# Kernel tuning notes

Hardware: AMD Instinct MI355X
Metric: run time of the kernel (lower is better)

The kernel has to match this reference:

```python
import jax, jax.numpy as jnp
import numpy as np

N_NODES = 1_000_000
N_EDGES = 16_000_000
ALPHA = 0.85
MAX_ITER = 100
TOL = 1e-6


def setup_inputs() -> dict:
    key = jax.random.key(0)
    k1, k2 = jax.random.split(key)
    x = jax.random.normal(k1, (N_NODES,), dtype=jnp.float32)
    edge_index = jax.random.randint(k2, (2, N_EDGES), 0, N_NODES, dtype=jnp.int64)
    return {"x": x, "edge_index": edge_index}


def reference(x, edge_index):
    N = x.shape[0]
    rows = edge_index[0]  # destination (row index of sparse M)
    cols = edge_index[1]  # source (column index; out-degree normalization)

    # values of M*alpha: alpha / out_degree(col), gathered per edge
    deg = jax.ops.segment_sum(jnp.ones_like(cols, dtype=jnp.float32), cols,
                              num_segments=N)  # torch.bincount(columns)
    vals = ALPHA / deg[cols]  # [E]; div-by-zero -> inf, matching torch

    inv_n = jnp.float32(1.0) / N
    teleport = (1.0 - ALPHA) * inv_n
    v0 = jnp.full((N,), inv_n, dtype=jnp.float32)
    thresh = jnp.float32(N) * TOL

    def step(carry, _):
        v, done = carry
        # SpMV: out[row] += vals * v[col]
        new_v = jax.ops.segment_sum(vals * v[cols], rows, num_segments=N) + teleport
        err = jnp.abs(new_v - v).sum()
        v_next = jnp.where(done, v, new_v)
        done_next = done | (err < thresh)
        return (v_next, done_next), None

    (v, _), _ = jax.lax.scan(step, (v0, jnp.array(False)), None, length=MAX_ITER)
    return v
```

## Files before the change

kernel.cpp:

```cpp
#include <hip/hip_runtime.h>
#include <hip/hip_cooperative_groups.h>

namespace cg = cooperative_groups;


static constexpr int   NN       = 1000000;
static constexpr int   NE       = 16000000;
static constexpr float ALPHA    = 0.85f;
static constexpr int   MAX_ITER = 100;
static constexpr float THRESH   = 1.0f;
static constexpr float INV_N    = 1.0f / 1000000.0f;
static constexpr float TELEPORT = 0.15f * (1.0f / 1000000.0f);
static constexpr float SCALE    = 8796093022208.0f;
static constexpr float INVSCALE = 1.0f / 8796093022208.0f;

static constexpr int T     = 256;
static constexpr int NCH   = 2048;
static constexpr int BSH   = 14;
static constexpr int BKN   = 16384;
static constexpr int NBK   = 64;
static constexpr int NSUBB = 496;
static constexpr int NSLC  = 489;

static constexpr size_t OFF_WCG  = 0;
static constexpr size_t OFF_COLP = 0;
static constexpr size_t OFF_HP   = 32001024;
static constexpr size_t OFF_WRG  = 64002048;
static constexpr size_t OFF_PACC = 96003072;
static constexpr size_t OFF_CNTR = 128508928;
static constexpr size_t OFF_CNTC = 129033216;
static constexpr size_t OFF_CTRL = 129557504;
static constexpr size_t OFF_RDEG = 129561600;
static constexpr size_t OFF_W    = 133561600;
static constexpr size_t NEED     = 137561632;

typedef int      vi4 __attribute__((ext_vector_type(4)));
typedef unsigned vu4 __attribute__((ext_vector_type(4)));

template<typename TT>
__device__ __forceinline__ TT ntload(const TT* p) { return __builtin_nontemporal_load(p); }

struct P {
    unsigned* wcg; unsigned short* colp; unsigned short* hpart; unsigned short* wrg;
    int* pacc; unsigned* cntR; unsigned* cntC;
    float* rdeg; float* w;
    unsigned* totR; unsigned* totC; unsigned* baseR; unsigned* baseC;
    unsigned* flags; int* ovf; float* errF;
};
__device__ __forceinline__ P mk(char* ws) {
    P p;
    p.wcg  = (unsigned*)(ws + OFF_WCG);
    p.colp = (unsigned short*)(ws + OFF_COLP);
    p.hpart= (unsigned short*)(ws + OFF_HP);
    p.wrg  = (unsigned short*)(ws + OFF_WRG);
    p.pacc = (int*)(ws + OFF_PACC);
    p.cntR = (unsigned*)(ws + OFF_CNTR);
    p.cntC = (unsigned*)(ws + OFF_CNTC);
    unsigned* ctrl = (unsigned*)(ws + OFF_CTRL);
    p.rdeg = (float*)(ws + OFF_RDEG);
    p.w    = (float*)(ws + OFF_W);
    p.totR = ctrl; p.totC = ctrl + 64; p.baseR = ctrl + 128; p.baseC = ctrl + 200;
    p.flags = ctrl + 280; p.ovf = (int*)(ctrl + 281); p.errF = (float*)(ctrl + 288);
    return p;
}

__device__ void atomic_fallback(cg::grid_group& grid, int is64,
                                const int* e32, const long long* e64,
                                int* ai, int* deg, float* rdeg,
                                float* vA, float* vB, float* w,
                                float* err, float* out,
                                int tid, int stride, int th)
{
    for (int i = tid; i < NN; i += stride) { ai[i] = 0; deg[i] = 0; vA[i] = INV_N; }
    grid.sync();
    if (is64) { const long long* cols = e64 + NE;
        for (int e = tid; e < NE; e += stride) atomicAdd(&deg[(int)cols[e]], 1); }
    else      { const int* cols = e32 + NE;
        for (int e = tid; e < NE; e += stride) atomicAdd(&deg[cols[e]], 1); }
    grid.sync();
    for (int i = tid; i < NN; i += stride) rdeg[i] = ALPHA / (float)deg[i];
    grid.sync();
    float* v = vA; float* nv = vB;
    for (int iter = 0; iter < MAX_ITER; ++iter) {
        for (int i = tid; i < NN; i += stride) { w[i] = v[i] * rdeg[i]; ai[i] = 0; }
        grid.sync();
        if (is64) { const long long* rows = e64; const long long* cols = e64 + NE;
            for (int e = tid; e < NE; e += stride)
                atomicAdd(&ai[(int)rows[e]], __float2int_rn(w[(int)cols[e]] * SCALE)); }
        else { const int* rows = e32; const int* cols = e32 + NE;
            for (int e = tid; e < NE; e += stride)
                atomicAdd(&ai[rows[e]], __float2int_rn(w[cols[e]] * SCALE)); }
        grid.sync();
        float pe = 0.0f;
        for (int i = tid; i < NN; i += stride) {
            float x = TELEPORT + (float)ai[i] * INVSCALE;
            pe += fabsf(x - v[i]); nv[i] = x;
        }
        #pragma unroll
        for (int off = 32; off > 0; off >>= 1) pe += __shfl_down(pe, off, 64);
        if ((th & 63) == 0) unsafeAtomicAdd(&err[iter], pe);
        grid.sync();
        float e = ((volatile float*)err)[iter];
        float* t = v; v = nv; nv = t;
        if (e < THRESH) break;
    }
    for (int i = tid; i < NN; i += stride) out[i] = v[i];
}

__global__ __launch_bounds__(256) void k0_init(const int* __restrict__ e32, char* ws)
{
    P p = mk(ws);
    __shared__ int snz;
    const int th = threadIdx.x;
    if (th == 0) snz = 0;
    __syncthreads();
    if (e32[2 * th + 1] != 0) atomicOr(&snz, 1);
    __syncthreads();
    if (th == 0) { p.flags[0] = (snz == 0) ? 1u : 0u; *p.ovf = 0; p.w[NN] = 0.0f; }
    if (th < MAX_ITER) p.errF[th] = 0.0f;
}

__global__ __launch_bounds__(256, 8) void k1_hist(const int* __restrict__ e32, char* ws)
{
    P p = mk(ws);
    if (p.flags[0]) return;
    __shared__ int h[128];
    const int th = threadIdx.x, blk = blockIdx.x;
    const int e0 = (int)(((long long)NE * blk) >> 11);
    const int e1 = (int)(((long long)NE * (blk + 1)) >> 11);
    if (th < 128) h[th] = 0;
    __syncthreads();
    const vi4* R4 = (const vi4*)e32;
    const vi4* C4 = (const vi4*)(e32 + NE);
    const int qe = (e1 + 3) >> 2;
    for (int q = (e0 >> 2) + th; q < qe; q += T) {
        vi4 R = R4[q], C = C4[q];
        int rr[4] = {R.x, R.y, R.z, R.w}, cc[4] = {C.x, C.y, C.z, C.w};
        #pragma unroll
        for (int j = 0; j < 4; ++j) {
            int e = 4 * q + j;
            if (e >= e0 && e < e1) {
                atomicAdd(&h[rr[j] >> BSH], 1);
                atomicAdd(&h[64 + (cc[j] >> BSH)], 1);
            }
        }
    }
    __syncthreads();
    if (th < 64) {
        p.cntR[(size_t)th * NCH + blk] = (unsigned)h[th];
        p.cntC[(size_t)th * NCH + blk] = (unsigned)h[64 + th];
    }
}

__global__ __launch_bounds__(256, 4) void k2_scan(char* ws)
{
    P p = mk(ws);
    if (p.flags[0]) return;
    __shared__ int S[256];
    const int th = threadIdx.x, blk = blockIdx.x;
    const int side = blk >> 6, b = blk & 63;
    unsigned* cnt = (side ? p.cntC : p.cntR) + (size_t)b * NCH;
    unsigned v[8]; unsigned s = 0;
    #pragma unroll
    for (int i = 0; i < 8; ++i) { v[i] = cnt[8 * th + i]; s += v[i]; }
    S[th] = (int)s; __syncthreads();
    for (int off = 1; off < 256; off <<= 1) {
        int x = (th >= off) ? S[th - off] : 0;
        __syncthreads(); S[th] += x; __syncthreads();
    }
    unsigned run = (unsigned)S[th] - s;
    #pragma unroll
    for (int i = 0; i < 8; ++i) { unsigned t = v[i]; cnt[8 * th + i] = run; run += t; }
    if (th == 255) (side ? p.totC : p.totR)[b] = run;
}

__global__ __launch_bounds__(256) void k2b_bases(char* ws)
{
    P p = mk(ws);
    if (p.flags[0]) return;
    __shared__ int S[128];
    const int th = threadIdx.x;
    unsigned pt = 0;
    if (th < 128) {
        unsigned t = (th < 64) ? p.totR[th] : p.totC[th - 64];
        pt = (t + 7u) & ~7u;
        S[th] = (int)pt;
    }
    __syncthreads();
    for (int off = 1; off < 64; off <<= 1) {
        int x = (th < 128 && (th & 63) >= off) ? S[th - off] : 0;
        __syncthreads(); if (th < 128) S[th] += x; __syncthreads();
    }
    if (th < 64) {
        p.baseR[th] = (unsigned)S[th] - pt;
        if (th == 63) p.baseR[64] = (unsigned)S[63];
    } else if (th < 128) {
        p.baseC[th - 64] = (unsigned)S[th] - pt;
        if (th == 127) p.baseC[64] = (unsigned)S[127];
    }
    __syncthreads();
    if (th < 64) {
        unsigned tot = p.totC[th], bs = p.baseC[th], pp = (tot + 7u) & ~7u;
        for (unsigned i = tot; i < pp; ++i) p.colp[bs + i] = 0;
    }
}

__global__ __launch_bounds__(256, 6) void k3a_col(const int* __restrict__ e32, char* ws)
{
    P p = mk(ws);
    if (p.flags[0]) return;
    __shared__ int SH3[4288];
    unsigned short* pcL = (unsigned short*)SH3;
    int* fills = SH3 + 4096; int* flsh = SH3 + 4160; int* wpos = SH3 + 4224;
    const int th = threadIdx.x, blk = blockIdx.x;
    if (th < 64) { fills[th] = 0; flsh[th] = 0;
                   wpos[th] = (int)(p.baseC[th] + p.cntC[(size_t)th * NCH + blk]); }
    __syncthreads();
    const int e0 = (int)(((long long)NE * blk) >> 11);
    const int e1 = (int)(((long long)NE * (blk + 1)) >> 11);
    const vi4* C4 = (const vi4*)(e32 + NE);
    const int qs = e0 >> 2, qe = (e1 + 3) >> 2;
    vi4 Ccur = {0, 0, 0, 0}; if (qs + th < qe) Ccur = C4[qs + th];
    for (int qb = qs; qb < qe; qb += T) {
        vi4 Cnext = {0, 0, 0, 0};
        { int qn = qb + T + th; if (qn < qe) Cnext = C4[qn]; }
        const int q = qb + th;
        if (q < qe) {
            int cc[4] = {Ccur.x, Ccur.y, Ccur.z, Ccur.w};
            #pragma unroll
            for (int j = 0; j < 4; ++j) {
                int e = 4 * q + j;
                if (e >= e0 && e < e1) {
                    int bb = cc[j] >> BSH;
                    int idx = atomicAdd(&fills[bb], 1);
                    pcL[bb * 128 + (idx & 127)] = (unsigned short)(cc[j] & (BKN - 1));
                }
            }
        }
        __syncthreads();
        const int wv = th >> 6, lane = th & 63;
        for (int k = 0; k < 16; ++k) {
            const int b = wv * 16 + k;
            int ff = fills[b], fl = flsh[b], wp = wpos[b];
            if (ff - fl > 128) *p.ovf = 1;
            while (ff - fl >= 64) {
                p.colp[wp + lane] = pcL[b * 128 + ((fl + lane) & 127)];
                fl += 64; wp += 64;
            }
            if (lane == 0) { flsh[b] = fl; wpos[b] = wp; }
        }
        __syncthreads();
        Ccur = Cnext;
    }
    {
        const int wv = th >> 6, lane = th & 63;
        for (int k = 0; k < 16; ++k) {
            const int b = wv * 16 + k;
            int ff = fills[b], fl = flsh[b], wp = wpos[b];
            while (ff > fl) {
                int n = min(64, ff - fl);
                if (lane < n) p.colp[wp + lane] = pcL[b * 128 + ((fl + lane) & 127)];
                fl += n; wp += n;
            }
        }
    }
}

__global__ __launch_bounds__(256, 2) void k4a_deg(char* ws)
{
    P p = mk(ws);
    if (p.flags[0] || *p.ovf) return;
    __shared__ int SH[16384];
    const int th = threadIdx.x, blk = blockIdx.x;
    const int b = blk >> 3, sub = blk & 7;
    for (int j = th; j < 16384; j += T) SH[j] = 0;
    __syncthreads();
    const unsigned bs = p.baseC[b], tot = p.totC[b], pt = (tot + 7u) & ~7u;
    const unsigned nq = pt >> 3;
    const unsigned qlo = (nq * (unsigned)sub) >> 3;
    const unsigned qhi = (nq * (unsigned)(sub + 1)) >> 3;
    const vu4* p8 = (const vu4*)p.colp + (bs >> 3);
    for (unsigned q = qlo + th; q < qhi; q += T) {
        vu4 x = ntload(p8 + q);
        atomicAdd(&SH[x.x & 0xFFFFu], 1); atomicAdd(&SH[x.x >> 16], 1);
        atomicAdd(&SH[x.y & 0xFFFFu], 1); atomicAdd(&SH[x.y >> 16], 1);
        atomicAdd(&SH[x.z & 0xFFFFu], 1); atomicAdd(&SH[x.z >> 16], 1);
        atomicAdd(&SH[x.w & 0xFFFFu], 1); atomicAdd(&SH[x.w >> 16], 1);
    }
    __syncthreads();
    unsigned* hp = (unsigned*)(p.hpart + (size_t)blk * 16384);
    for (int j = th; j < 8192; j += T)
        __builtin_nontemporal_store(
            (unsigned)((SH[2*j] & 0xFFFF) | (SH[2*j+1] << 16)), hp + j);
}

__global__ __launch_bounds__(256, 8) void k4b_merge(char* ws)
{
    P p = mk(ws);
    if (p.flags[0] || *p.ovf) return;
    const int th = threadIdx.x, blk = blockIdx.x;
    const int b = blk >> 3, off = (blk & 7) * 2048;
    const unsigned padC = ((p.totC[b] + 7u) & ~7u) - p.totC[b];
    for (int j = th; j < 1024; j += T) {
        unsigned lo = 0, hi = 0;
        #pragma unroll
        for (int q = 0; q < 8; ++q) {
            const unsigned* hp = (const unsigned*)(p.hpart + (size_t)(b*8+q)*16384 + off);
            unsigned x = ntload(hp + j);
            lo += x & 0xFFFFu; hi += x >> 16;
        }
        if (off == 0 && j == 0) lo -= padC;
        int node = b * BKN + off + 2 * j;
        if (node < NN) {
            float r0 = ALPHA / (float)(int)lo;
            float r1 = ALPHA / (float)(int)hi;
            float2 rr = {r0, r1};
            *(float2*)&p.rdeg[node] = rr;
            float2 ww = {INV_N * r0, INV_N * r1};
            *(float2*)&p.w[node] = ww;
        }
    }
}

__global__ __launch_bounds__(256, 3) void k3b_row(const int* __restrict__ e32, char* ws)
{
    P p = mk(ws);
    if (p.flags[0] || *p.ovf) return;
    __shared__ int SH3[12480];
    int*            wcL = SH3;
    unsigned short* wrL = (unsigned short*)(SH3 + 8192);
    int* fills = SH3 + 12288; int* flsh = SH3 + 12352; int* wpos = SH3 + 12416;
    const int th = threadIdx.x, blk = blockIdx.x;
    if (blk < 64 && th == 0) {
        unsigned tot = p.totR[blk], bs = p.baseR[blk], pt = (tot + 7u) & ~7u;
        for (unsigned i = tot; i < pt; ++i) { p.wcg[bs + i] = (unsigned)NN; p.wrg[bs + i] = 0; }
    }
    if (th < 64) { fills[th] = 0; flsh[th] = 0;
                   wpos[th] = (int)(p.baseR[th] + p.cntR[(size_t)th * NCH + blk]); }
    __syncthreads();
    const int e0 = (int)(((long long)NE * blk) >> 11);
    const int e1 = (int)(((long long)NE * (blk + 1)) >> 11);
    const vi4* R4 = (const vi4*)e32;
    const vi4* C4 = (const vi4*)(e32 + NE);
    const int qs = e0 >> 2, qe = (e1 + 3) >> 2;
    vi4 Rcur = {0,0,0,0}, Ccur = {0,0,0,0};
    if (qs + th < qe) { Rcur = R4[qs + th]; Ccur = C4[qs + th]; }
    for (int qb = qs; qb < qe; qb += T) {
        vi4 Rnext = {0,0,0,0}, Cnext = {0,0,0,0};
        { int qn = qb + T + th; if (qn < qe) { Rnext = R4[qn]; Cnext = C4[qn]; } }
        const int q = qb + th;
        if (q < qe) {
            int rr[4] = {Rcur.x, Rcur.y, Rcur.z, Rcur.w};
            int cc[4] = {Ccur.x, Ccur.y, Ccur.z, Ccur.w};
            #pragma unroll
            for (int j = 0; j < 4; ++j) {
                int e = 4 * q + j;
                if (e >= e0 && e < e1) {
                    int bb = rr[j] >> BSH;
                    int idx = atomicAdd(&fills[bb], 1);
                    int sl = idx & 127;
                    wcL[bb * 128 + sl] = cc[j];
                    wrL[bb * 128 + sl] = (unsigned short)(rr[j] & (BKN - 1));
                }
            }
        }
        __syncthreads();
        const int wv = th >> 6, lane = th & 63;
        for (int k = 0; k < 16; ++k) {
            const int b = wv * 16 + k;
            int ff = fills[b], fl = flsh[b], wp = wpos[b];
            if (ff - fl > 128) *p.ovf = 1;
            while (ff - fl >= 64) {
                p.wcg[wp + lane] = (unsigned)wcL[b * 128 + ((fl + lane) & 127)];
                p.wrg[wp + lane] = wrL[b * 128 + ((fl + lane) & 127)];
                fl += 64; wp += 64;
            }
            if (lane == 0) { flsh[b] = fl; wpos[b] = wp; }
        }
        __syncthreads();
        Rcur = Rnext; Ccur = Cnext;
    }
    {
        const int wv = th >> 6, lane = th & 63;
        for (int k = 0; k < 16; ++k) {
            const int b = wv * 16 + k;
            int ff = fills[b], fl = flsh[b], wp = wpos[b];
            while (ff > fl) {
                int n = min(64, ff - fl);
                if (lane < n) {
                    p.wcg[wp + lane] = (unsigned)wcL[b * 128 + ((fl + lane) & 127)];
                    p.wrg[wp + lane] = wrL[b * 128 + ((fl + lane) & 127)];
                }
                fl += n; wp += n;
            }
        }
    }
}

__global__ __launch_bounds__(256, 2)
void k5_iter(const int* __restrict__ e32, const long long* __restrict__ e64,
             char* __restrict__ ws, float* __restrict__ out)
{
    cg::grid_group grid = cg::this_grid();
    P p = mk(ws);
    const int th = threadIdx.x, blk = blockIdx.x;
    const int tid = blk * T + th;
    const int stride = gridDim.x * T;
    __shared__ int SH[16384];
    __shared__ float sred[4];

    if (p.flags[0] || *p.ovf) {
        atomic_fallback(grid, (int)p.flags[0], e32, e64,
                        (int*)ws, (int*)(ws + (size_t)4*1024*1024), p.rdeg,
                        (float*)(ws + (size_t)8*1024*1024),
                        (float*)(ws + (size_t)12*1024*1024),
                        (float*)(ws + (size_t)16*1024*1024),
                        p.errF, out, tid, stride, th);
        return;
    }

    for (int iter = 0; iter < MAX_ITER; ++iter) {
        if (blk < NSUBB) {
            const int b = blk >> 3, sub = blk & 7;
            for (int j = th; j < 16384; j += T) SH[j] = 0;
            __syncthreads();
            const unsigned bs = p.baseR[b], tot = p.totR[b], pt = (tot + 7u) & ~7u;
            const unsigned nq = pt >> 3;
            const unsigned qlo = (nq * (unsigned)sub) >> 3;
            const unsigned qhi = (nq * (unsigned)(sub + 1)) >> 3;
            const vu4* r8 = (const vu4*)p.wrg + (bs >> 3);
            const vi4* c8 = (const vi4*)p.wcg + (bs >> 2);
            for (unsigned q = qlo + th; q < qhi; q += T) {
                vu4 rl = ntload(r8 + q);
                vi4 ca = ntload(c8 + 2*q), cb = ntload(c8 + 2*q + 1);
                atomicAdd(&SH[rl.x & 0xFFFFu], __float2int_rn(p.w[(unsigned)ca.x] * SCALE));
                atomicAdd(&SH[rl.x >> 16],     __float2int_rn(p.w[(unsigned)ca.y] * SCALE));
                atomicAdd(&SH[rl.y & 0xFFFFu], __float2int_rn(p.w[(unsigned)ca.z] * SCALE));
                atomicAdd(&SH[rl.y >> 16],     __float2int_rn(p.w[(unsigned)ca.w] * SCALE));
                atomicAdd(&SH[rl.z & 0xFFFFu], __float2int_rn(p.w[(unsigned)cb.x] * SCALE));
                atomicAdd(&SH[rl.z >> 16],     __float2int_rn(p.w[(unsigned)cb.y] * SCALE));
                atomicAdd(&SH[rl.w & 0xFFFFu], __float2int_rn(p.w[(unsigned)cb.z] * SCALE));
                atomicAdd(&SH[rl.w >> 16],     __float2int_rn(p.w[(unsigned)cb.w] * SCALE));
            }
            __syncthreads();
            vi4* pa = (vi4*)(p.pacc + (size_t)blk * 16384);
            const vi4* s4 = (const vi4*)SH;
            for (int j = th; j < 4096; j += T)
                __builtin_nontemporal_store(s4[j], pa + j);
        }
        grid.sync();

        float pe = 0.0f;
        if (blk < NSLC) {
            const int b = blk >> 3, off = (blk & 7) * 2048;
            for (int g = th; g < 512; g += T) {
                int node = b * BKN + off + 4 * g;
                if (node < NN) {
                    vi4 acc = {0, 0, 0, 0};
                    #pragma unroll
                    for (int q = 0; q < 8; ++q) {
                        const vi4* pp = (const vi4*)(p.pacc + (size_t)(b*8+q)*16384 + off);
                        vi4 x = ntload(pp + g);
                        acc.x += x.x; acc.y += x.y; acc.z += x.z; acc.w += x.w;
                    }
                    float x0 = TELEPORT + (float)acc.x * INVSCALE;
                    float x1 = TELEPORT + (float)acc.y * INVSCALE;
                    float x2 = TELEPORT + (float)acc.z * INVSCALE;
                    float x3 = TELEPORT + (float)acc.w * INVSCALE;
                    float4 prev;
                    if (iter == 0) prev = make_float4(INV_N, INV_N, INV_N, INV_N);
                    else           prev = *(const float4*)&out[node];
                    pe += fabsf(x0 - prev.x) + fabsf(x1 - prev.y)
                        + fabsf(x2 - prev.z) + fabsf(x3 - prev.w);
                    float4 nv = {x0, x1, x2, x3};
                    *(float4*)&out[node] = nv;
                    float4 rd = *(const float4*)&p.rdeg[node];
                    float4 nw = {x0*rd.x, x1*rd.y, x2*rd.z, x3*rd.w};
                    *(float4*)&p.w[node] = nw;
                }
            }
            #pragma unroll
            for (int o2 = 32; o2 > 0; o2 >>= 1) pe += __shfl_down(pe, o2, 64);
            if ((th & 63) == 0) sred[th >> 6] = pe;
            __syncthreads();
            if (th == 0)
                unsafeAtomicAdd(&p.errF[iter], sred[0] + sred[1] + sred[2] + sred[3]);
        }
        grid.sync();
        const float e = ((volatile float*)p.errF)[iter];
        if (e < THRESH) break;
    }
}

__global__ __launch_bounds__(256, 4)
void pagerank_atomic(const int* __restrict__ e32, const long long* __restrict__ e64,
                     int* __restrict__ ai, int* __restrict__ deg,
                     float* __restrict__ rdeg, float* __restrict__ vA,
                     float* __restrict__ vB, float* __restrict__ w,
                     float* __restrict__ err, int* __restrict__ flags,
                     float* __restrict__ out)
{
    cg::grid_group grid = cg::this_grid();
    const int tid = blockIdx.x * blockDim.x + threadIdx.x;
    const int stride = gridDim.x * blockDim.x;
    if (tid < MAX_ITER) err[tid] = 0.0f;
    if (tid == 0) {
        int nz = 0;
        for (int k = 1; k < 512; k += 2) nz |= e32[k];
        flags[0] = (nz == 0) ? 1 : 0;
    }
    grid.sync();
    atomic_fallback(grid, flags[0], e32, e64, ai, deg, rdeg, vA, vB, w, err, out,
                    tid, stride, threadIdx.x);
}

extern "C" void kernel_launch(void* const* d_in, const int* in_sizes, int n_in,
                              void* d_out, int out_size, void* d_ws, size_t ws_size,
                              hipStream_t stream)
{
    (void)n_in; (void)out_size; (void)in_sizes;
    const int*       e32 = (const int*)d_in[1];
    const long long* e64 = (const long long*)d_in[1];
    float* out = (float*)d_out;
    char*  ws  = (char*)d_ws;

    int occ = 0;
    hipOccupancyMaxActiveBlocksPerMultiprocessor(&occ, (const void*)k5_iter, T, 0);

    if (ws_size >= NEED && occ >= 2) {
        k0_init<<<1,    T, 0, stream>>>(e32, ws);
        k1_hist<<<NCH,  T, 0, stream>>>(e32, ws);
        k2_scan<<<128,  T, 0, stream>>>(ws);
        k2b_bases<<<1,  T, 0, stream>>>(ws);
        k3a_col<<<NCH,  T, 0, stream>>>(e32, ws);
        k4a_deg<<<NSUBB,T, 0, stream>>>(ws);
        k4b_merge<<<NSLC,T,0, stream>>>(ws);
        k3b_row<<<NCH,  T, 0, stream>>>(e32, ws);
        void* args[] = { (void*)&e32, (void*)&e64, (void*)&ws, (void*)&out };
        hipLaunchCooperativeKernel((const void*)k5_iter,
                                   dim3(512), dim3(T), args, 0, stream);
        return;
    }

    const size_t MB = 1024 * 1024;
    int*   ai    = (int*)(ws);
    int*   deg   = (int*)(ws + 4 * MB);
    float* rdeg  = (float*)(ws + 8 * MB);
    float* vA    = (float*)(ws + 12 * MB);
    float* vB    = (float*)(ws + 16 * MB);
    float* w     = (float*)(ws + 20 * MB);
    float* err   = (float*)(ws + 24 * MB);
    int*   flg   = (int*)(ws + 24 * MB + 4096);
    int occ2 = 0;
    hipOccupancyMaxActiveBlocksPerMultiprocessor(&occ2, (const void*)pagerank_atomic, 256, 0);
    if (occ2 < 1) occ2 = 1;
    int grid = occ2 * 256; if (grid > 2048) grid = 2048;
    void* args[] = { (void*)&e32, (void*)&e64, (void*)&ai, (void*)&deg, (void*)&rdeg,
                     (void*)&vA, (void*)&vB, (void*)&w, (void*)&err, (void*)&flg,
                     (void*)&out };
    hipLaunchCooperativeKernel((const void*)pagerank_atomic,
                               dim3(grid), dim3(256), args, 0, stream);
}
```

Baseline: 618.3 us.

## Compute out-degrees with global atomics and software-pipeline the SpMV gather loop

Replaces the multi-kernel column bucketing pipeline (column partitioning, per-bucket shared histograms and a merge) with direct global atomicAdd on a per-node degree array during the histogram pass, followed by a small kernel that turns the counts into reciprocal degrees and the initial weights. It also software-pipelines the SpMV inner loop in the iteration kernel, double-buffering the index loads and the w gathers so the gathers of the next chunk overlap the shared-memory atomics of the current one. Global atomics on 16M random addresses may contend or generate heavy memory traffic, and the pipelining raises register pressure in a kernel launched with occupancy bound 2.

```diff
diff --git a/kernel.cpp b/kernel.cpp
--- a/kernel.cpp
+++ b/kernel.cpp
@@ -21,10 +21,10 @@
 static constexpr int NBK   = 64;
 static constexpr int NSUBB = 496;
 static constexpr int NSLC  = 489;
+static constexpr int NDEG4 = 250000;
+static constexpr int GDEG  = 977;
 
 static constexpr size_t OFF_WCG  = 0;
-static constexpr size_t OFF_COLP = 0;
-static constexpr size_t OFF_HP   = 32001024;
 static constexpr size_t OFF_WRG  = 64002048;
 static constexpr size_t OFF_PACC = 96003072;
 static constexpr size_t OFF_CNTR = 128508928;
@@ -41,7 +41,7 @@
 __device__ __forceinline__ TT ntload(const TT* p) { return __builtin_nontemporal_load(p); }
 
 struct P {
-    unsigned* wcg; unsigned short* colp; unsigned short* hpart; unsigned short* wrg;
+    unsigned* wcg; unsigned short* wrg;
     int* pacc; unsigned* cntR; unsigned* cntC;
     float* rdeg; float* w;
     unsigned* totR; unsigned* totC; unsigned* baseR; unsigned* baseC;
@@ -50,8 +50,6 @@
 __device__ __forceinline__ P mk(char* ws) {
     P p;
     p.wcg  = (unsigned*)(ws + OFF_WCG);
-    p.colp = (unsigned short*)(ws + OFF_COLP);
-    p.hpart= (unsigned short*)(ws + OFF_HP);
     p.wrg  = (unsigned short*)(ws + OFF_WRG);
     p.pacc = (int*)(ws + OFF_PACC);
     p.cntR = (unsigned*)(ws + OFF_CNTR);
@@ -112,23 +110,31 @@
     P p = mk(ws);
     __shared__ int snz;
     const int th = threadIdx.x;
-    if (th == 0) snz = 0;
-    __syncthreads();
-    if (e32[2 * th + 1] != 0) atomicOr(&snz, 1);
-    __syncthreads();
-    if (th == 0) { p.flags[0] = (snz == 0) ? 1u : 0u; *p.ovf = 0; p.w[NN] = 0.0f; }
-    if (th < MAX_ITER) p.errF[th] = 0.0f;
+    const int idx = blockIdx.x * T + th;
+    if (idx < NDEG4) {
+        vi4 z = {0, 0, 0, 0};
+        *((vi4*)(ws + OFF_RDEG) + idx) = z;
+    }
+    if (blockIdx.x == 0) {
+        if (th == 0) snz = 0;
+        __syncthreads();
+        if (e32[2 * th + 1] != 0) atomicOr(&snz, 1);
+        __syncthreads();
+        if (th == 0) { p.flags[0] = (snz == 0) ? 1u : 0u; *p.ovf = 0; p.w[NN] = 0.0f; }
+        if (th < MAX_ITER) p.errF[th] = 0.0f;
+    }
 }
 
 __global__ __launch_bounds__(256, 8) void k1_hist(const int* __restrict__ e32, char* ws)
 {
     P p = mk(ws);
     if (p.flags[0]) return;
-    __shared__ int h[128];
+    __shared__ int h[64];
+    int* __restrict__ deg = (int*)(ws + OFF_RDEG);
     const int th = threadIdx.x, blk = blockIdx.x;
     const int e0 = (int)(((long long)NE * blk) >> 11);
     const int e1 = (int)(((long long)NE * (blk + 1)) >> 11);
-    if (th < 128) h[th] = 0;
+    if (th < 64) h[th] = 0;
     __syncthreads();
     const vi4* R4 = (const vi4*)e32;
     const vi4* C4 = (const vi4*)(e32 + NE);
@@ -141,15 +147,12 @@
             int e = 4 * q + j;
             if (e >= e0 && e < e1) {
                 atomicAdd(&h[rr[j] >> BSH], 1);
-                atomicAdd(&h[64 + (cc[j] >> BSH)], 1);
+                atomicAdd(&deg[cc[j]], 1);
             }
         }
     }
     __syncthreads();
-    if (th < 64) {
-        p.cntR[(size_t)th * NCH + blk] = (unsigned)h[th];
-        p.cntC[(size_t)th * NCH + blk] = (unsigned)h[64 + th];
-    }
+    if (th < 64) p.cntR[(size_t)th * NCH + blk] = (unsigned)h[th];
 }
 
 __global__ __launch_bounds__(256, 4) void k2_scan(char* ws)
@@ -157,9 +160,8 @@
     P p = mk(ws);
     if (p.flags[0]) return;
     __shared__ int S[256];
-    const int th = threadIdx.x, blk = blockIdx.x;
-    const int side = blk >> 6, b = blk & 63;
-    unsigned* cnt = (side ? p.cntC : p.cntR) + (size_t)b * NCH;
+    const int th = threadIdx.x, b = blockIdx.x;
+    unsigned* cnt = p.cntR + (size_t)b * NCH;
     unsigned v[8]; unsigned s = 0;
     #pragma unroll
     for (int i = 0; i < 8; ++i) { v[i] = cnt[8 * th + i]; s += v[i]; }
@@ -171,155 +173,47 @@
     unsigned run = (unsigned)S[th] - s;
     #pragma unroll
     for (int i = 0; i < 8; ++i) { unsigned t = v[i]; cnt[8 * th + i] = run; run += t; }
-    if (th == 255) (side ? p.totC : p.totR)[b] = run;
+    if (th == 255) p.totR[b] = run;
 }
 
 __global__ __launch_bounds__(256) void k2b_bases(char* ws)
 {
     P p = mk(ws);
     if (p.flags[0]) return;
-    __shared__ int S[128];
+    __shared__ int S[64];
     const int th = threadIdx.x;
     unsigned pt = 0;
-    if (th < 128) {
-        unsigned t = (th < 64) ? p.totR[th] : p.totC[th - 64];
+    if (th < 64) {
+        unsigned t = p.totR[th];
         pt = (t + 7u) & ~7u;
         S[th] = (int)pt;
     }
     __syncthreads();
     for (int off = 1; off < 64; off <<= 1) {
-        int x = (th < 128 && (th & 63) >= off) ? S[th - off] : 0;
-        __syncthreads(); if (th < 128) S[th] += x; __syncthreads();
+        int x = (th < 64 && th >= off) ? S[th - off] : 0;
+        __syncthreads(); if (th < 64) S[th] += x; __syncthreads();
     }
     if (th < 64) {
         p.baseR[th] = (unsigned)S[th] - pt;
         if (th == 63) p.baseR[64] = (unsigned)S[63];
-    } else if (th < 128) {
-        p.baseC[th - 64] = (unsigned)S[th] - pt;
-        if (th == 127) p.baseC[64] = (unsigned)S[127];
-    }
-    __syncthreads();
-    if (th < 64) {
-        unsigned tot = p.totC[th], bs = p.baseC[th], pp = (tot + 7u) & ~7u;
-        for (unsigned i = tot; i < pp; ++i) p.colp[bs + i] = 0;
-    }
-}
-
-__global__ __launch_bounds__(256, 6) void k3a_col(const int* __restrict__ e32, char* ws)
+    }
+}
+
+__global__ __launch_bounds__(256) void k2c_rdeg(char* ws)
 {
     P p = mk(ws);
     if (p.flags[0]) return;
-    __shared__ int SH3[4288];
-    unsigned short* pcL = (unsigned short*)SH3;
-    int* fills = SH3 + 4096; int* flsh = SH3 + 4160; int* wpos = SH3 + 4224;
-    const int th = threadIdx.x, blk = blockIdx.x;
-    if (th < 64) { fills[th] = 0; flsh[th] = 0;
-                   wpos[th] = (int)(p.baseC[th] + p.cntC[(size_t)th * NCH + blk]); }
-    __syncthreads();
-    const int e0 = (int)(((long long)NE * blk) >> 11);
-    const int e1 = (int)(((long long)NE * (blk + 1)) >> 11);
-    const vi4* C4 = (const vi4*)(e32 + NE);
-    const int qs = e0 >> 2, qe = (e1 + 3) >> 2;
-    vi4 Ccur = {0, 0, 0, 0}; if (qs + th < qe) Ccur = C4[qs + th];
-    for (int qb = qs; qb < qe; qb += T) {
-        vi4 Cnext = {0, 0, 0, 0};
-        { int qn = qb + T + th; if (qn < qe) Cnext = C4[qn]; }
-        const int q = qb + th;
-        if (q < qe) {
-            int cc[4] = {Ccur.x, Ccur.y, Ccur.z, Ccur.w};
-            #pragma unroll
-            for (int j = 0; j < 4; ++j) {
-                int e = 4 * q + j;
-                if (e >= e0 && e < e1) {
-                    int bb = cc[j] >> BSH;
-                    int idx = atomicAdd(&fills[bb], 1);
-                    pcL[bb * 128 + (idx & 127)] = (unsigned short)(cc[j] & (BKN - 1));
-                }
-            }
-        }
-        __syncthreads();
-        const int wv = th >> 6, lane = th & 63;
-        for (int k = 0; k < 16; ++k) {
-            const int b = wv * 16 + k;
-            int ff = fills[b], fl = flsh[b], wp = wpos[b];
-            if (ff - fl > 128) *p.ovf = 1;
-            while (ff - fl >= 64) {
-                p.colp[wp + lane] = pcL[b * 128 + ((fl + lane) & 127)];
-                fl += 64; wp += 64;
-            }
-            if (lane == 0) { flsh[b] = fl; wpos[b] = wp; }
-        }
-        __syncthreads();
-        Ccur = Cnext;
-    }
-    {
-        const int wv = th >> 6, lane = th & 63;
-        for (int k = 0; k < 16; ++k) {
-            const int b = wv * 16 + k;
-            int ff = fills[b], fl = flsh[b], wp = wpos[b];
-            while (ff > fl) {
-                int n = min(64, ff - fl);
-                if (lane < n) p.colp[wp + lane] = pcL[b * 128 + ((fl + lane) & 127)];
-                fl += n; wp += n;
-            }
-        }
-    }
-}
-
-__global__ __launch_bounds__(256, 2) void k4a_deg(char* ws)
-{
-    P p = mk(ws);
-    if (p.flags[0] || *p.ovf) return;
-    __shared__ int SH[16384];
-    const int th = threadIdx.x, blk = blockIdx.x;
-    const int b = blk >> 3, sub = blk & 7;
-    for (int j = th; j < 16384; j += T) SH[j] = 0;
-    __syncthreads();
-    const unsigned bs = p.baseC[b], tot = p.totC[b], pt = (tot + 7u) & ~7u;
-    const unsigned nq = pt >> 3;
-    const unsigned qlo = (nq * (unsigned)sub) >> 3;
-    const unsigned qhi = (nq * (unsigned)(sub + 1)) >> 3;
-    const vu4* p8 = (const vu4*)p.colp + (bs >> 3);
-    for (unsigned q = qlo + th; q < qhi; q += T) {
-        vu4 x = ntload(p8 + q);
-        atomicAdd(&SH[x.x & 0xFFFFu], 1); atomicAdd(&SH[x.x >> 16], 1);
-        atomicAdd(&SH[x.y & 0xFFFFu], 1); atomicAdd(&SH[x.y >> 16], 1);
-        atomicAdd(&SH[x.z & 0xFFFFu], 1); atomicAdd(&SH[x.z >> 16], 1);
-        atomicAdd(&SH[x.w & 0xFFFFu], 1); atomicAdd(&SH[x.w >> 16], 1);
-    }
-    __syncthreads();
-    unsigned* hp = (unsigned*)(p.hpart + (size_t)blk * 16384);
-    for (int j = th; j < 8192; j += T)
-        __builtin_nontemporal_store(
-            (unsigned)((SH[2*j] & 0xFFFF) | (SH[2*j+1] << 16)), hp + j);
-}
-
-__global__ __launch_bounds__(256, 8) void k4b_merge(char* ws)
-{
-    P p = mk(ws);
-    if (p.flags[0] || *p.ovf) return;
-    const int th = threadIdx.x, blk = blockIdx.x;
-    const int b = blk >> 3, off = (blk & 7) * 2048;
-    const unsigned padC = ((p.totC[b] + 7u) & ~7u) - p.totC[b];
-    for (int j = th; j < 1024; j += T) {
-        unsigned lo = 0, hi = 0;
-        #pragma unroll
-        for (int q = 0; q < 8; ++q) {
-            const unsigned* hp = (const unsigned*)(p.hpart + (size_t)(b*8+q)*16384 + off);
-            unsigned x = ntload(hp + j);
-            lo += x & 0xFFFFu; hi += x >> 16;
-        }
-        if (off == 0 && j == 0) lo -= padC;
-        int node = b * BKN + off + 2 * j;
-        if (node < NN) {
-            float r0 = ALPHA / (float)(int)lo;
-            float r1 = ALPHA / (float)(int)hi;
-            float2 rr = {r0, r1};
-            *(float2*)&p.rdeg[node] = rr;
-            float2 ww = {INV_N * r0, INV_N * r1};
-            *(float2*)&p.w[node] = ww;
-        }
-    }
+    const int idx = blockIdx.x * T + threadIdx.x;
+    if (idx >= NDEG4) return;
+    const vi4 d = *((const vi4*)(const void*)p.rdeg + idx);
+    float4 r;
+    r.x = ALPHA / (float)d.x;
+    r.y = ALPHA / (float)d.y;
+    r.z = ALPHA / (float)d.z;
+    r.w = ALPHA / (float)d.w;
+    *((float4*)p.rdeg + idx) = r;
+    float4 w0 = {INV_N * r.x, INV_N * r.y, INV_N * r.z, INV_N * r.w};
+    *((float4*)p.w + idx) = w0;
 }
 
 __global__ __launch_bounds__(256, 3) void k3b_row(const int* __restrict__ e32, char* ws)
@@ -397,6 +291,22 @@
     }
 }
 
+#define GATH(G, CA, CB)                              \
+    G##0 = w[(unsigned)CA.x]; G##1 = w[(unsigned)CA.y]; \
+    G##2 = w[(unsigned)CA.z]; G##3 = w[(unsigned)CA.w]; \
+    G##4 = w[(unsigned)CB.x]; G##5 = w[(unsigned)CB.y]; \
+    G##6 = w[(unsigned)CB.z]; G##7 = w[(unsigned)CB.w];
+
+#define ATOM(RL, G)                                                         \
+    atomicAdd(&SH[RL.x & 0xFFFFu], __float2int_rn(G##0 * SCALE));           \
+    atomicAdd(&SH[RL.x >> 16],     __float2int_rn(G##1 * SCALE));           \
+    atomicAdd(&SH[RL.y & 0xFFFFu], __float2int_rn(G##2 * SCALE));           \
+    atomicAdd(&SH[RL.y >> 16],     __float2int_rn(G##3 * SCALE));           \
+    atomicAdd(&SH[RL.z & 0xFFFFu], __float2int_rn(G##4 * SCALE));           \
+    atomicAdd(&SH[RL.z >> 16],     __float2int_rn(G##5 * SCALE));           \
+    atomicAdd(&SH[RL.w & 0xFFFFu], __float2int_rn(G##6 * SCALE));           \
+    atomicAdd(&SH[RL.w >> 16],     __float2int_rn(G##7 * SCALE));
+
 __global__ __launch_bounds__(256, 2)
 void k5_iter(const int* __restrict__ e32, const long long* __restrict__ e64,
              char* __restrict__ ws, float* __restrict__ out)
@@ -428,19 +338,28 @@
             const unsigned nq = pt >> 3;
             const unsigned qlo = (nq * (unsigned)sub) >> 3;
             const unsigned qhi = (nq * (unsigned)(sub + 1)) >> 3;
-            const vu4* r8 = (const vu4*)p.wrg + (bs >> 3);
-            const vi4* c8 = (const vi4*)p.wcg + (bs >> 2);
-            for (unsigned q = qlo + th; q < qhi; q += T) {
-                vu4 rl = ntload(r8 + q);
-                vi4 ca = ntload(c8 + 2*q), cb = ntload(c8 + 2*q + 1);
-                atomicAdd(&SH[rl.x & 0xFFFFu], __float2int_rn(p.w[(unsigned)ca.x] * SCALE));
-                atomicAdd(&SH[rl.x >> 16],     __float2int_rn(p.w[(unsigned)ca.y] * SCALE));
-                atomicAdd(&SH[rl.y & 0xFFFFu], __float2int_rn(p.w[(unsigned)ca.z] * SCALE));
-                atomicAdd(&SH[rl.y >> 16],     __float2int_rn(p.w[(unsigned)ca.w] * SCALE));
-                atomicAdd(&SH[rl.z & 0xFFFFu], __float2int_rn(p.w[(unsigned)cb.x] * SCALE));
-                atomicAdd(&SH[rl.z >> 16],     __float2int_rn(p.w[(unsigned)cb.y] * SCALE));
-                atomicAdd(&SH[rl.w & 0xFFFFu], __float2int_rn(p.w[(unsigned)cb.z] * SCALE));
-                atomicAdd(&SH[rl.w >> 16],     __float2int_rn(p.w[(unsigned)cb.w] * SCALE));
+            const vu4* __restrict__ r8 = (const vu4*)p.wrg + (bs >> 3);
+            const vi4* __restrict__ c8 = (const vi4*)p.wcg + (bs >> 2);
+            const float* __restrict__ w = p.w;
+
+            unsigned q = qlo + th;
+            vu4 rlA = {0,0,0,0}, rlB = {0,0,0,0}, rgA = {0,0,0,0}, rgB = {0,0,0,0};
+            vi4 caA = {0,0,0,0}, cbA = {0,0,0,0}, caB = {0,0,0,0}, cbB = {0,0,0,0};
+            float gA0=0,gA1=0,gA2=0,gA3=0,gA4=0,gA5=0,gA6=0,gA7=0;
+            float gB0=0,gB1=0,gB2=0,gB3=0,gB4=0,gB5=0,gB6=0,gB7=0;
+            if (q < qhi)     { rlA = r8[q];     caA = c8[2*q];       cbA = c8[2*q+1]; }
+            if (q + T < qhi) { rlB = r8[q+T];   caB = c8[2*(q+T)];   cbB = c8[2*(q+T)+1]; }
+            if (q < qhi)     { GATH(gA, caA, cbA); rgA = rlA; }
+            while (q < qhi) {
+                if (q + T < qhi)   { GATH(gB, caB, cbB); rgB = rlB; }
+                if (q + 2*T < qhi) { rlA = r8[q+2*T]; caA = c8[2*(q+2*T)]; cbA = c8[2*(q+2*T)+1]; }
+                ATOM(rgA, gA);
+                q += T;
+                if (q >= qhi) break;
+                if (q + T < qhi)   { GATH(gA, caA, cbA); rgA = rlA; }
+                if (q + 2*T < qhi) { rlB = r8[q+2*T]; caB = c8[2*(q+2*T)]; cbB = c8[2*(q+2*T)+1]; }
+                ATOM(rgB, gB);
+                q += T;
             }
             __syncthreads();
             vi4* pa = (vi4*)(p.pacc + (size_t)blk * 16384);
@@ -458,8 +377,8 @@
                 if (node < NN) {
                     vi4 acc = {0, 0, 0, 0};
                     #pragma unroll
-                    for (int q = 0; q < 8; ++q) {
-                        const vi4* pp = (const vi4*)(p.pacc + (size_t)(b*8+q)*16384 + off);
+                    for (int qq = 0; qq < 8; ++qq) {
+                        const vi4* pp = (const vi4*)(p.pacc + (size_t)(b*8+qq)*16384 + off);
                         vi4 x = ntload(pp + g);
                         acc.x += x.x; acc.y += x.y; acc.z += x.z; acc.w += x.w;
                     }
@@ -528,13 +447,11 @@
     hipOccupancyMaxActiveBlocksPerMultiprocessor(&occ, (const void*)k5_iter, T, 0);
 
     if (ws_size >= NEED && occ >= 2) {
-        k0_init<<<1,    T, 0, stream>>>(e32, ws);
+        k0_init<<<GDEG, T, 0, stream>>>(e32, ws);
         k1_hist<<<NCH,  T, 0, stream>>>(e32, ws);
-        k2_scan<<<128,  T, 0, stream>>>(ws);
+        k2_scan<<<64,   T, 0, stream>>>(ws);
         k2b_bases<<<1,  T, 0, stream>>>(ws);
-        k3a_col<<<NCH,  T, 0, stream>>>(e32, ws);
-        k4a_deg<<<NSUBB,T, 0, stream>>>(ws);
-        k4b_merge<<<NSLC,T,0, stream>>>(ws);
+        k2c_rdeg<<<GDEG,T, 0, stream>>>(ws);
         k3b_row<<<NCH,  T, 0, stream>>>(e32, ws);
         void* args[] = { (void*)&e32, (void*)&e64, (void*)&ws, (void*)&out };
         hipLaunchCooperativeKernel((const void*)k5_iter,
```

New measurement: 1.098 ms. 1.78x slower.

## Software-pipeline SpMV gathers and fuse degree count into one kernel

Applied to the files above, without the earlier changes.

The per-iteration SpMV loop is reworked into a two-stage software pipeline: edge index loads run two strides ahead and the w[] gathers one stride ahead of the shared-memory atomics, so more memory latency stays in flight. Nontemporal loads on the edge stream are dropped in favour of plain loads. Separately, the degree histogram is computed with one block per bucket that writes rdeg and w directly, removing the partial-histogram buffer and the merge kernel. The cost is higher register pressure in the cooperative kernel and much less parallelism in the degree stage, since only 62 blocks each scan a whole bucket.

```diff
diff --git a/kernel.cpp b/kernel.cpp
--- a/kernel.cpp
+++ b/kernel.cpp
@@ -19,12 +19,12 @@
 static constexpr int BSH   = 14;
 static constexpr int BKN   = 16384;
 static constexpr int NBK   = 64;
+static constexpr int NBKU  = 62;
 static constexpr int NSUBB = 496;
 static constexpr int NSLC  = 489;
 
 static constexpr size_t OFF_WCG  = 0;
 static constexpr size_t OFF_COLP = 0;
-static constexpr size_t OFF_HP   = 32001024;
 static constexpr size_t OFF_WRG  = 64002048;
 static constexpr size_t OFF_PACC = 96003072;
 static constexpr size_t OFF_CNTR = 128508928;
@@ -41,7 +41,7 @@
 __device__ __forceinline__ TT ntload(const TT* p) { return __builtin_nontemporal_load(p); }
 
 struct P {
-    unsigned* wcg; unsigned short* colp; unsigned short* hpart; unsigned short* wrg;
+    unsigned* wcg; unsigned short* colp; unsigned short* wrg;
     int* pacc; unsigned* cntR; unsigned* cntC;
     float* rdeg; float* w;
     unsigned* totR; unsigned* totC; unsigned* baseR; unsigned* baseC;
@@ -51,7 +51,6 @@
     P p;
     p.wcg  = (unsigned*)(ws + OFF_WCG);
     p.colp = (unsigned short*)(ws + OFF_COLP);
-    p.hpart= (unsigned short*)(ws + OFF_HP);
     p.wrg  = (unsigned short*)(ws + OFF_WRG);
     p.pacc = (int*)(ws + OFF_PACC);
     p.cntR = (unsigned*)(ws + OFF_CNTR);
@@ -266,21 +265,18 @@
     }
 }
 
-__global__ __launch_bounds__(256, 2) void k4a_deg(char* ws)
+__global__ __launch_bounds__(256, 2) void k4_deg(char* ws)
 {
     P p = mk(ws);
     if (p.flags[0] || *p.ovf) return;
     __shared__ int SH[16384];
-    const int th = threadIdx.x, blk = blockIdx.x;
-    const int b = blk >> 3, sub = blk & 7;
+    const int th = threadIdx.x, b = blockIdx.x;
     for (int j = th; j < 16384; j += T) SH[j] = 0;
     __syncthreads();
     const unsigned bs = p.baseC[b], tot = p.totC[b], pt = (tot + 7u) & ~7u;
     const unsigned nq = pt >> 3;
-    const unsigned qlo = (nq * (unsigned)sub) >> 3;
-    const unsigned qhi = (nq * (unsigned)(sub + 1)) >> 3;
     const vu4* p8 = (const vu4*)p.colp + (bs >> 3);
-    for (unsigned q = qlo + th; q < qhi; q += T) {
+    for (unsigned q = th; q < nq; q += T) {
         vu4 x = ntload(p8 + q);
         atomicAdd(&SH[x.x & 0xFFFFu], 1); atomicAdd(&SH[x.x >> 16], 1);
         atomicAdd(&SH[x.y & 0xFFFFu], 1); atomicAdd(&SH[x.y >> 16], 1);
@@ -288,36 +284,19 @@
         atomicAdd(&SH[x.w & 0xFFFFu], 1); atomicAdd(&SH[x.w >> 16], 1);
     }
     __syncthreads();
-    unsigned* hp = (unsigned*)(p.hpart + (size_t)blk * 16384);
-    for (int j = th; j < 8192; j += T)
-        __builtin_nontemporal_store(
-            (unsigned)((SH[2*j] & 0xFFFF) | (SH[2*j+1] << 16)), hp + j);
-}
-
-__global__ __launch_bounds__(256, 8) void k4b_merge(char* ws)
-{
-    P p = mk(ws);
-    if (p.flags[0] || *p.ovf) return;
-    const int th = threadIdx.x, blk = blockIdx.x;
-    const int b = blk >> 3, off = (blk & 7) * 2048;
-    const unsigned padC = ((p.totC[b] + 7u) & ~7u) - p.totC[b];
-    for (int j = th; j < 1024; j += T) {
-        unsigned lo = 0, hi = 0;
-        #pragma unroll
-        for (int q = 0; q < 8; ++q) {
-            const unsigned* hp = (const unsigned*)(p.hpart + (size_t)(b*8+q)*16384 + off);
-            unsigned x = ntload(hp + j);
-            lo += x & 0xFFFFu; hi += x >> 16;
-        }
-        if (off == 0 && j == 0) lo -= padC;
-        int node = b * BKN + off + 2 * j;
+    if (th == 0) SH[0] -= (int)(pt - tot);
+    __syncthreads();
+    for (int g = th; g < 4096; g += T) {
+        int node = b * BKN + 4 * g;
         if (node < NN) {
-            float r0 = ALPHA / (float)(int)lo;
-            float r1 = ALPHA / (float)(int)hi;
-            float2 rr = {r0, r1};
-            *(float2*)&p.rdeg[node] = rr;
-            float2 ww = {INV_N * r0, INV_N * r1};
-            *(float2*)&p.w[node] = ww;
+            float r0 = ALPHA / (float)SH[4*g+0];
+            float r1 = ALPHA / (float)SH[4*g+1];
+            float r2 = ALPHA / (float)SH[4*g+2];
+            float r3 = ALPHA / (float)SH[4*g+3];
+            float4 rr = {r0, r1, r2, r3};
+            *(float4*)&p.rdeg[node] = rr;
+            float4 ww = {INV_N * r0, INV_N * r1, INV_N * r2, INV_N * r3};
+            *(float4*)&p.w[node] = ww;
         }
     }
 }
@@ -397,6 +376,22 @@
     }
 }
 
+#define GATH(G, CA, CB)                              \
+    G##0 = w[(unsigned)CA.x]; G##1 = w[(unsigned)CA.y]; \
+    G##2 = w[(unsigned)CA.z]; G##3 = w[(unsigned)CA.w]; \
+    G##4 = w[(unsigned)CB.x]; G##5 = w[(unsigned)CB.y]; \
+    G##6 = w[(unsigned)CB.z]; G##7 = w[(unsigned)CB.w];
+
+#define ATOM(RL, G)                                                         \
+    atomicAdd(&SH[RL.x & 0xFFFFu], __float2int_rn(G##0 * SCALE));           \
+    atomicAdd(&SH[RL.x >> 16],     __float2int_rn(G##1 * SCALE));           \
+    atomicAdd(&SH[RL.y & 0xFFFFu], __float2int_rn(G##2 * SCALE));           \
+    atomicAdd(&SH[RL.y >> 16],     __float2int_rn(G##3 * SCALE));           \
+    atomicAdd(&SH[RL.z & 0xFFFFu], __float2int_rn(G##4 * SCALE));           \
+    atomicAdd(&SH[RL.z >> 16],     __float2int_rn(G##5 * SCALE));           \
+    atomicAdd(&SH[RL.w & 0xFFFFu], __float2int_rn(G##6 * SCALE));           \
+    atomicAdd(&SH[RL.w >> 16],     __float2int_rn(G##7 * SCALE));
+
 __global__ __launch_bounds__(256, 2)
 void k5_iter(const int* __restrict__ e32, const long long* __restrict__ e64,
              char* __restrict__ ws, float* __restrict__ out)
@@ -428,19 +423,28 @@
             const unsigned nq = pt >> 3;
             const unsigned qlo = (nq * (unsigned)sub) >> 3;
             const unsigned qhi = (nq * (unsigned)(sub + 1)) >> 3;
-            const vu4* r8 = (const vu4*)p.wrg + (bs >> 3);
-            const vi4* c8 = (const vi4*)p.wcg + (bs >> 2);
-            for (unsigned q = qlo + th; q < qhi; q += T) {
-                vu4 rl = ntload(r8 + q);
-                vi4 ca = ntload(c8 + 2*q), cb = ntload(c8 + 2*q + 1);
-                atomicAdd(&SH[rl.x & 0xFFFFu], __float2int_rn(p.w[(unsigned)ca.x] * SCALE));
-                atomicAdd(&SH[rl.x >> 16],     __float2int_rn(p.w[(unsigned)ca.y] * SCALE));
-                atomicAdd(&SH[rl.y & 0xFFFFu], __float2int_rn(p.w[(unsigned)ca.z] * SCALE));
-                atomicAdd(&SH[rl.y >> 16],     __float2int_rn(p.w[(unsigned)ca.w] * SCALE));
-                atomicAdd(&SH[rl.z & 0xFFFFu], __float2int_rn(p.w[(unsigned)cb.x] * SCALE));
-                atomicAdd(&SH[rl.z >> 16],     __float2int_rn(p.w[(unsigned)cb.y] * SCALE));
-                atomicAdd(&SH[rl.w & 0xFFFFu], __float2int_rn(p.w[(unsigned)cb.z] * SCALE));
-                atomicAdd(&SH[rl.w >> 16],     __float2int_rn(p.w[(unsigned)cb.w] * SCALE));
+            const vu4* __restrict__ r8 = (const vu4*)p.wrg + (bs >> 3);
+            const vi4* __restrict__ c8 = (const vi4*)p.wcg + (bs >> 2);
+            const float* __restrict__ w = p.w;
+
+            unsigned q = qlo + th;
+            vu4 rlA = {0,0,0,0}, rlB = {0,0,0,0}, rgA = {0,0,0,0}, rgB = {0,0,0,0};
+            vi4 caA = {0,0,0,0}, cbA = {0,0,0,0}, caB = {0,0,0,0}, cbB = {0,0,0,0};
+            float gA0=0,gA1=0,gA2=0,gA3=0,gA4=0,gA5=0,gA6=0,gA7=0;
+            float gB0=0,gB1=0,gB2=0,gB3=0,gB4=0,gB5=0,gB6=0,gB7=0;
+            if (q < qhi)     { rlA = r8[q];     caA = c8[2*q];       cbA = c8[2*q+1]; }
+            if (q + T < qhi) { rlB = r8[q+T];   caB = c8[2*(q+T)];   cbB = c8[2*(q+T)+1]; }
+            if (q < qhi)     { GATH(gA, caA, cbA); rgA = rlA; }
+            while (q < qhi) {
+                if (q + T < qhi)   { GATH(gB, caB, cbB); rgB = rlB; }
+                if (q + 2*T < qhi) { rlA = r8[q+2*T]; caA = c8[2*(q+2*T)]; cbA = c8[2*(q+2*T)+1]; }
+                ATOM(rgA, gA);
+                q += T;
+                if (q >= qhi) break;
+                if (q + T < qhi)   { GATH(gA, caA, cbA); rgA = rlA; }
+                if (q + 2*T < qhi) { rlB = r8[q+2*T]; caB = c8[2*(q+2*T)]; cbB = c8[2*(q+2*T)+1]; }
+                ATOM(rgB, gB);
+                q += T;
             }
             __syncthreads();
             vi4* pa = (vi4*)(p.pacc + (size_t)blk * 16384);
@@ -458,8 +462,8 @@
                 if (node < NN) {
                     vi4 acc = {0, 0, 0, 0};
                     #pragma unroll
-                    for (int q = 0; q < 8; ++q) {
-                        const vi4* pp = (const vi4*)(p.pacc + (size_t)(b*8+q)*16384 + off);
+                    for (int qq = 0; qq < 8; ++qq) {
+                        const vi4* pp = (const vi4*)(p.pacc + (size_t)(b*8+qq)*16384 + off);
                         vi4 x = ntload(pp + g);
                         acc.x += x.x; acc.y += x.y; acc.z += x.z; acc.w += x.w;
                     }
@@ -533,8 +537,7 @@
         k2_scan<<<128,  T, 0, stream>>>(ws);
         k2b_bases<<<1,  T, 0, stream>>>(ws);
         k3a_col<<<NCH,  T, 0, stream>>>(e32, ws);
-        k4a_deg<<<NSUBB,T, 0, stream>>>(ws);
-        k4b_merge<<<NSLC,T,0, stream>>>(ws);
+        k4_deg<<<NBKU,  T, 0, stream>>>(ws);
         k3b_row<<<NCH,  T, 0, stream>>>(e32, ws);
         void* args[] = { (void*)&e32, (void*)&e64, (void*)&ws, (void*)&out };
         hipLaunchCooperativeKernel((const void*)k5_iter,
```

New measurement: 645.6 us. +4.4%, slower.
